# Optimization experiments

Measured on AMD Instinct MI355X. Metric: run time of the kernel, lower is better.

## Reference

```python
import jax, jax.numpy as jnp
import numpy as np

B, M_IN, N_OUT = 131072, 64, 64


def setup_inputs() -> dict:
    key = jax.random.key(0)
    k1, k2, k3 = jax.random.split(key, 3)
    x = jax.random.normal(k1, (B, M_IN, 4), dtype=jnp.float32)
    x = x.at[:, :, 0].set(0.0)  # pure quaternion input (w-component = 0)
    stdv_w = (2.0 / (M_IN + N_OUT)) ** 0.5
    W_q = jax.random.normal(k2, (N_OUT, M_IN, 4), dtype=jnp.float32) * (stdv_w / 2.0)
    theta_q = jax.random.normal(k3, (N_OUT, 4), dtype=jnp.float32) * 0.01
    theta_q = theta_q.at[:, 0].set(0.0)  # pure quaternion threshold
    return {"x_batch": x, "W_q": W_q, "theta_q": theta_q}


def _hamilton_sum(x, W):
    """s[b,n] = sum_m W[n,m] (x) x[b,m]  (Hamilton product, W on the left).
    x: (B, M, 4), W: (N, M, 4) -> (B, N, 4)"""
    ww, wx, wy, wz = (W[..., i] for i in range(4))   # each (N, M)
    xw, xx, xy, xz = (x[..., i] for i in range(4))   # each (B, M)
    dot = lambda p, q: jnp.einsum('bm,nm->bn', p, q)
    sw = dot(xw, ww) - dot(xx, wx) - dot(xy, wy) - dot(xz, wz)
    sx = dot(xx, ww) + dot(xw, wx) + dot(xz, wy) - dot(xy, wz)
    sy = dot(xy, ww) - dot(xz, wx) + dot(xw, wy) + dot(xx, wz)
    sz = dot(xz, ww) + dot(xy, wx) - dot(xx, wy) + dot(xw, wz)
    return jnp.stack([sw, sx, sy, sz], axis=-1)


def reference(x_batch, W_q, theta_q):
    # Isokawa quaternion neuron: s = sum_m W (x) x - theta; y = sigmoid(s) per component.
    s = _hamilton_sum(x_batch, W_q) - theta_q[None, :, :]  # (B, N, 4) pre-activation (s_internal)
    return jax.nn.sigmoid(s)
```

## Files before the change

### kernel.cpp

```cpp
#include <hip/hip_runtime.h>
#include <hip/hip_bf16.h>


typedef __bf16 bf16_t;
typedef bf16_t bf16x8 __attribute__((ext_vector_type(8)));
typedef bf16_t bf16x4v __attribute__((ext_vector_type(4)));
typedef float f32x4 __attribute__((ext_vector_type(4)));

#define B_TOTAL 131072
#define KDIM 256
#define NDIM 256
#define ROWS 64
#define THREADS 512
#define LDS_STRIDE 264

__global__ void coef_kernel(const float* __restrict__ W, bf16_t* __restrict__ coef) {
    const int widx[4][4] = {{0,1,2,3},{1,0,3,2},{2,3,0,1},{3,2,1,0}};
    const float sgn[4][4] = {{1.f,-1.f,-1.f,-1.f},
                             {1.f, 1.f,-1.f, 1.f},
                             {1.f, 1.f, 1.f,-1.f},
                             {1.f,-1.f, 1.f, 1.f}};
    int g = blockIdx.x * blockDim.x + threadIdx.x;
#pragma unroll
    for (int e = 0; e < 4; e++) {
        int F = g * 4 + e;
        int j    = F & 7;
        int lane = (F >> 3) & 63;
        int ks   = (F >> 9) & 7;
        int nt   = F >> 12;
        int col  = nt * 16 + (lane & 15);
        int k    = ks * 32 + (lane >> 4) * 8 + j;
        int n = col >> 2, oc = col & 3;
        int m = k >> 2,   ic = k & 3;
        float v = sgn[oc][ic] * W[n * 256 + m * 4 + widx[oc][ic]];
        coef[F] = (bf16_t)v;
    }
}

__global__ __launch_bounds__(THREADS, 4)
void main_kernel(const float* __restrict__ x, const bf16x8* __restrict__ coef,
                 const float* __restrict__ theta, float* __restrict__ out) {
    __shared__ __align__(16) bf16_t xs[ROWS * LDS_STRIDE];

    const int tid  = threadIdx.x;
    const int tile = blockIdx.x;
    const int row0 = tile * ROWS;

    const float4* xp = (const float4*)(x + (long)row0 * KDIM);
    float4 v[8];
#pragma unroll
    for (int i = 0; i < 8; i++) v[i] = xp[tid + THREADS * i];
#pragma unroll
    for (int i = 0; i < 8; i++) {
        int f = tid + THREADS * i;
        int r = f >> 6;
        int c = (f & 63) * 4;
        bf16x4v w;
        w.x = (bf16_t)v[i].x; w.y = (bf16_t)v[i].y;
        w.z = (bf16_t)v[i].z; w.w = (bf16_t)v[i].w;
        *(bf16x4v*)&xs[r * LDS_STRIDE + c] = w;
    }
    __syncthreads();

    const int wave = tid >> 6, lane = tid & 63;
    const int colq = wave & 3, rowh = wave >> 2;
    const int l15  = lane & 15, quad = lane >> 4;

    float th[4];
#pragma unroll
    for (int ct = 0; ct < 4; ct++) th[ct] = theta[colq * 64 + ct * 16 + l15];

    f32x4 acc[2][4];
#pragma unroll
    for (int rt = 0; rt < 2; rt++)
#pragma unroll
        for (int ct = 0; ct < 4; ct++) acc[rt][ct] = (f32x4)(0.f);

#pragma unroll 2
    for (int ks = 0; ks < 8; ks++) {
        bf16x8 a[2], b[4];
#pragma unroll
        for (int rt = 0; rt < 2; rt++) {
            int r = rowh * 32 + rt * 16 + l15;
            a[rt] = *(const bf16x8*)&xs[r * LDS_STRIDE + ks * 32 + quad * 8];
        }
#pragma unroll
        for (int ct = 0; ct < 4; ct++) {
            int nt = colq * 4 + ct;
            b[ct] = coef[(nt * 8 + ks) * 64 + lane];
        }
#pragma unroll
        for (int rt = 0; rt < 2; rt++)
#pragma unroll
            for (int ct = 0; ct < 4; ct++)
                acc[rt][ct] = __builtin_amdgcn_mfma_f32_16x16x32_bf16(
                    a[rt], b[ct], acc[rt][ct], 0, 0, 0);
    }

#pragma unroll
    for (int rt = 0; rt < 2; rt++) {
        int rbase = row0 + rowh * 32 + rt * 16 + quad * 4;
#pragma unroll
        for (int ct = 0; ct < 4; ct++) {
            int col = colq * 64 + ct * 16 + l15;
#pragma unroll
            for (int r = 0; r < 4; r++) {
                float s = acc[rt][ct][r] - th[ct];
                float y = 1.0f / (1.0f + __expf(-s));
                out[(long)(rbase + r) * NDIM + col] = y;
            }
        }
    }
}

extern "C" void kernel_launch(void* const* d_in, const int* in_sizes, int n_in,
                              void* d_out, int out_size, void* d_ws, size_t ws_size,
                              hipStream_t stream) {
    const float* x     = (const float*)d_in[0];
    const float* W     = (const float*)d_in[1];
    const float* theta = (const float*)d_in[2];
    float* out = (float*)d_out;
    bf16_t* coef = (bf16_t*)d_ws;

    if (ws_size < 65536 * sizeof(bf16_t)) return;

    coef_kernel<<<64, 256, 0, stream>>>(W, coef);
    main_kernel<<<B_TOTAL / ROWS, THREADS, 0, stream>>>(
        x, (const bf16x8*)coef, theta, out);
}
```

Measured before the change: 250.2 us.

## Remap waves to column strips and preload B fragments into registers

The wave-to-output mapping changes: each of the 8 waves now owns a 32-column strip across all 64 rows, where before each had a 64-column by 32-row tile. All 16 coefficient fragments for that strip are loaded into registers up front, overlapping the x tile load and removing the global coefficient loads from the inner k-loop. The k-loop is fully unrolled and does 4 LDS A-reads per step instead of 2. The coef kernel is also changed to one element per thread over more blocks. The cost is more registers per thread and more LDS traffic, which could limit occupancy.

```diff
diff --git a/kernel.cpp b/kernel.cpp
--- a/kernel.cpp
+++ b/kernel.cpp
@@ -20,21 +20,16 @@
                              {1.f, 1.f,-1.f, 1.f},
                              {1.f, 1.f, 1.f,-1.f},
                              {1.f,-1.f, 1.f, 1.f}};
-    int g = blockIdx.x * blockDim.x + threadIdx.x;
-#pragma unroll
-    for (int e = 0; e < 4; e++) {
-        int F = g * 4 + e;
-        int j    = F & 7;
-        int lane = (F >> 3) & 63;
-        int ks   = (F >> 9) & 7;
-        int nt   = F >> 12;
-        int col  = nt * 16 + (lane & 15);
-        int k    = ks * 32 + (lane >> 4) * 8 + j;
-        int n = col >> 2, oc = col & 3;
-        int m = k >> 2,   ic = k & 3;
-        float v = sgn[oc][ic] * W[n * 256 + m * 4 + widx[oc][ic]];
-        coef[F] = (bf16_t)v;
-    }
+    int F = blockIdx.x * blockDim.x + threadIdx.x;
+    int j    = F & 7;
+    int lane = (F >> 3) & 63;
+    int ks   = (F >> 9) & 7;
+    int nt   = F >> 12;
+    int col  = nt * 16 + (lane & 15);
+    int k    = ks * 32 + (lane >> 4) * 8 + j;
+    int n = col >> 2, oc = col & 3;
+    int m = k >> 2,   ic = k & 3;
+    coef[F] = (bf16_t)(sgn[oc][ic] * W[n * 256 + m * 4 + widx[oc][ic]]);
 }
 
 __global__ __launch_bounds__(THREADS, 4)
@@ -43,13 +38,22 @@
     __shared__ __align__(16) bf16_t xs[ROWS * LDS_STRIDE];
 
     const int tid  = threadIdx.x;
-    const int tile = blockIdx.x;
-    const int row0 = tile * ROWS;
+    const int row0 = blockIdx.x * ROWS;
+    const int wave = tid >> 6, lane = tid & 63;
+    const int l15  = lane & 15, quad = lane >> 4;
 
     const float4* xp = (const float4*)(x + (long)row0 * KDIM);
     float4 v[8];
 #pragma unroll
     for (int i = 0; i < 8; i++) v[i] = xp[tid + THREADS * i];
+
+    bf16x8 breg[2][8];
+#pragma unroll
+    for (int ct = 0; ct < 2; ct++)
+#pragma unroll
+        for (int ks = 0; ks < 8; ks++)
+            breg[ct][ks] = coef[((wave * 2 + ct) * 8 + ks) * 64 + lane];
+
 #pragma unroll
     for (int i = 0; i < 8; i++) {
         int f = tid + THREADS * i;
@@ -62,47 +66,36 @@
     }
     __syncthreads();
 
-    const int wave = tid >> 6, lane = tid & 63;
-    const int colq = wave & 3, rowh = wave >> 2;
-    const int l15  = lane & 15, quad = lane >> 4;
+    f32x4 acc[4][2];
+#pragma unroll
+    for (int rt = 0; rt < 4; rt++)
+#pragma unroll
+        for (int ct = 0; ct < 2; ct++) acc[rt][ct] = (f32x4)(0.f);
 
-    float th[4];
 #pragma unroll
-    for (int ct = 0; ct < 4; ct++) th[ct] = theta[colq * 64 + ct * 16 + l15];
-
-    f32x4 acc[2][4];
+    for (int ks = 0; ks < 8; ks++) {
+        bf16x8 a[4];
 #pragma unroll
-    for (int rt = 0; rt < 2; rt++)
+        for (int rt = 0; rt < 4; rt++)
+            a[rt] = *(const bf16x8*)&xs[(rt * 16 + l15) * LDS_STRIDE + ks * 32 + quad * 8];
 #pragma unroll
-        for (int ct = 0; ct < 4; ct++) acc[rt][ct] = (f32x4)(0.f);
-
-#pragma unroll 2
-    for (int ks = 0; ks < 8; ks++) {
-        bf16x8 a[2], b[4];
+        for (int rt = 0; rt < 4; rt++)
 #pragma unroll
-        for (int rt = 0; rt < 2; rt++) {
-            int r = rowh * 32 + rt * 16 + l15;
-            a[rt] = *(const bf16x8*)&xs[r * LDS_STRIDE + ks * 32 + quad * 8];
-        }
-#pragma unroll
-        for (int ct = 0; ct < 4; ct++) {
-            int nt = colq * 4 + ct;
-            b[ct] = coef[(nt * 8 + ks) * 64 + lane];
-        }
-#pragma unroll
-        for (int rt = 0; rt < 2; rt++)
-#pragma unroll
-            for (int ct = 0; ct < 4; ct++)
+            for (int ct = 0; ct < 2; ct++)
                 acc[rt][ct] = __builtin_amdgcn_mfma_f32_16x16x32_bf16(
-                    a[rt], b[ct], acc[rt][ct], 0, 0, 0);
+                    a[rt], breg[ct][ks], acc[rt][ct], 0, 0, 0);
     }
 
+    float th[2];
 #pragma unroll
-    for (int rt = 0; rt < 2; rt++) {
-        int rbase = row0 + rowh * 32 + rt * 16 + quad * 4;
+    for (int ct = 0; ct < 2; ct++) th[ct] = theta[wave * 32 + ct * 16 + l15];
+
 #pragma unroll
-        for (int ct = 0; ct < 4; ct++) {
-            int col = colq * 64 + ct * 16 + l15;
+    for (int rt = 0; rt < 4; rt++) {
+        int rbase = row0 + rt * 16 + quad * 4;
+#pragma unroll
+        for (int ct = 0; ct < 2; ct++) {
+            int col = wave * 32 + ct * 16 + l15;
 #pragma unroll
             for (int r = 0; r < 4; r++) {
                 float s = acc[rt][ct][r] - th[ct];
@@ -124,7 +117,7 @@
 
     if (ws_size < 65536 * sizeof(bf16_t)) return;
 
-    coef_kernel<<<64, 256, 0, stream>>>(W, coef);
+    coef_kernel<<<256, 256, 0, stream>>>(W, coef);
     main_kernel<<<B_TOTAL / ROWS, THREADS, 0, stream>>>(
         x, (const bf16x8*)coef, theta, out);
 }
```

After: 242.9 us. 1.03x faster.
